# Kernel optimization log

Hardware: AMD Instinct MI355X
Metric: run time of the kernel (lower is better)

The kernel has to match this reference:

```python
import jax, jax.numpy as jnp
import numpy as np

N = 50000          # nodes
E_RAND = 800000    # random edges (avg degree 16)
D_IN = 128
H = 4              # heads (both layers)
C = 64             # per-head channels (both layers)
NEG_SLOPE = 0.2    # PyG GATConv default leaky_relu slope


def _gat_conv(x, src, dst, W, att_src, att_dst, bias, concat):
    """PyG GATConv (dropout=0, self-loops already in edge list).
    x:[N,Din] W:[Din,H*C] att_*:[H,C] bias:[H*C] or [C]."""
    n = x.shape[0]
    h = (x @ W).reshape(n, H, C)                      # [N,H,C]
    a_src = jnp.sum(h * att_src, axis=-1)             # [N,H]
    a_dst = jnp.sum(h * att_dst, axis=-1)             # [N,H]
    e = jax.nn.leaky_relu(a_src[src] + a_dst[dst], NEG_SLOPE)  # [E,H]
    # segment softmax over incoming edges of each destination node
    m = jax.ops.segment_max(e, dst, num_segments=n)    # [N,H]
    e = jnp.exp(e - m[dst])
    denom = jax.ops.segment_sum(e, dst, num_segments=n)
    alpha = e / (denom[dst] + 1e-16)                   # [E,H]
    msg = h[src] * alpha[..., None]                    # [E,H,C]
    out = jax.ops.segment_sum(msg, dst, num_segments=n)  # [N,H,C]
    if concat:
        out = out.reshape(n, H * C)
    else:
        out = out.mean(axis=1)
    return out + bias


def setup_inputs() -> dict:
    key = jax.random.key(0)
    ks = jax.random.split(key, 10)
    x = jax.random.normal(ks[0], (N, D_IN), jnp.float32)
    src = jax.random.randint(ks[1], (E_RAND,), 0, N)
    dst = jax.random.randint(ks[2], (E_RAND,), 0, N)
    loops = jnp.arange(N)  # add_self_loops=True (PyG default)
    edge_index = jnp.stack([jnp.concatenate([src, loops]),
                            jnp.concatenate([dst, loops])]).astype(jnp.int32)
    g = lambda k, shp, fan: (jax.random.normal(k, shp, jnp.float32) / np.float32(np.sqrt(fan)))
    W1 = g(ks[3], (D_IN, H * C), D_IN)
    att_src1 = g(ks[4], (H, C), C)
    att_dst1 = g(ks[5], (H, C), C)
    b1 = jnp.zeros((H * C,), jnp.float32)
    W2 = g(ks[6], (H * C, H * C), H * C)
    att_src2 = g(ks[7], (H, C), C)
    att_dst2 = g(ks[8], (H, C), C)
    b2 = jnp.zeros((C,), jnp.float32)
    return {"x": x, "edge_index": edge_index,
            "W1": W1, "att_src1": att_src1, "att_dst1": att_dst1, "b1": b1,
            "W2": W2, "att_src2": att_src2, "att_dst2": att_dst2, "b2": b2}


def reference(x, edge_index, W1, att_src1, att_dst1, b1, W2, att_src2, att_dst2, b2):
    src, dst = edge_index[0], edge_index[1]
    h = jax.nn.relu(_gat_conv(x, src, dst, W1, att_src1, att_dst1, b1, concat=True))
    h = jax.nn.relu(_gat_conv(h, src, dst, W2, att_src2, att_dst2, b2, concat=False))
    return jax.nn.softmax(h, axis=1)
```

## Files before the change

kernel.cpp:

```cpp
#include <hip/hip_runtime.h>


typedef __attribute__((ext_vector_type(8))) short short8;
typedef __attribute__((ext_vector_type(4))) float f32x4;
typedef __attribute__((ext_vector_type(2))) float f32x2;

static __device__ __forceinline__ ushort f2bf(float f) {
  uint u = __float_as_uint(f);
  return (ushort)((u + 0x7FFFu + ((u >> 16) & 1u)) >> 16);
}
static __device__ __forceinline__ float bf2f(ushort s) {
  return __uint_as_float(((uint)s) << 16);
}
static __device__ __forceinline__ unsigned char f2fp8(float f) {
  int p = __builtin_amdgcn_cvt_pk_fp8_f32(f, f, 0, false);
  return (unsigned char)(p & 0xFF);
}
static __device__ __forceinline__ uint4 cvt8bf(const float4& a, const float4& b) {
  uint4 hh;
  hh.x = (uint)f2bf(a.x) | ((uint)f2bf(a.y) << 16);
  hh.y = (uint)f2bf(a.z) | ((uint)f2bf(a.w) << 16);
  hh.z = (uint)f2bf(b.x) | ((uint)f2bf(b.y) << 16);
  hh.w = (uint)f2bf(b.z) | ((uint)f2bf(b.w) << 16);
  return hh;
}
static __device__ __forceinline__ void gl16(const ushort* g, ushort* l) {
  __builtin_amdgcn_global_load_lds(
      (const __attribute__((address_space(1))) uint*)(g),
      (__attribute__((address_space(3))) uint*)(l), 16, 0, 0);
}

__global__ __launch_bounds__(256)
void k_prep(const float* __restrict__ W1, const float* __restrict__ W2,
            ushort* __restrict__ w1t, ushort* __restrict__ w2t,
            const float* __restrict__ x, ushort* __restrict__ xb,
            int* __restrict__ cnt, int N,
            int ng , int xcb) {
  const int b = blockIdx.x;
  if (b < 128) {
    int gid = b * 256 + threadIdx.x;
    int c = gid & 255, k = gid >> 8;
    w1t[(size_t)c * 128 + k] = f2bf(W1[(size_t)k * 256 + c]);
  } else if (b < 384) {
    int gid = (b - 128) * 256 + threadIdx.x;
    int c = gid & 255, k = gid >> 8;
    w2t[(size_t)c * 256 + k] = f2bf(W2[(size_t)k * 256 + c]);
  } else if (b < 384 + xcb) {
    int i = (b - 384) * 256 + threadIdx.x;
    if (i < ng) {
      const float4* xp = (const float4*)x + (size_t)i * 2;
      float4 a = xp[0], bb = xp[1];
      ((uint4*)xb)[i] = cvt8bf(a, bb);
    }
  } else {
    int i = (b - 384 - xcb) * 1024 + threadIdx.x;
#pragma unroll
    for (int k = 0; k < 4; k++) {
      int j = i + k * 256;
      if (j < N) cnt[j] = 0;
    }
  }
}

template <int K>
static __device__ __forceinline__
void gemm_body(int bid, const ushort* __restrict__ Ah,
               const ushort* __restrict__ Bt,
               unsigned char* __restrict__ hout, int Nrows,
               const float* __restrict__ att_s, const float* __restrict__ att_d,
               float* __restrict__ a_s, float* __restrict__ a_d) {
  __shared__ ushort Asb[2][128][32];
  __shared__ ushort Bhb[2][128][32];

  const int nrb = (Nrows + 127) >> 7;
  const int rb = (bid >> 4) * 8 + (bid & 7);
  const int ch = (bid >> 3) & 1;
  if (rb >= nrb) return;
  const int row0 = rb * 128;
  const int col0 = ch * 128;

  const int t = threadIdx.x;
  const int lane = t & 63;
  const int w = t >> 6;
  const int wr = (w >> 1) * 64;
  const int wc = (w & 1) * 64;
  const int fr = lane & 15;
  const int fq = lane >> 4;

  const int srow = lane >> 2;
  const int skc = (lane & 3) * 8;
  int ar0 = row0 + w * 32 + srow;
  int ar1 = ar0 + 16;
  ar0 = ar0 < Nrows ? ar0 : Nrows - 1;
  ar1 = ar1 < Nrows ? ar1 : Nrows - 1;
  const ushort* agp0 = Ah + (size_t)ar0 * K + skc;
  const ushort* agp1 = Ah + (size_t)ar1 * K + skc;
  const ushort* bhg0 = Bt + (size_t)(col0 + w * 32 + srow) * K + skc;
  const ushort* bhg1 = bhg0 + (size_t)16 * K;

  f32x4 acc[4][4] = {};

  auto stage = [&](int buf, int k0) {
    gl16(agp0 + k0, &Asb[buf][w * 32][0]);
    gl16(agp1 + k0, &Asb[buf][w * 32 + 16][0]);
    gl16(bhg0 + k0, &Bhb[buf][w * 32][0]);
    gl16(bhg1 + k0, &Bhb[buf][w * 32 + 16][0]);
  };

  stage(0, 0);
  const int NK = K / 32;
#pragma unroll
  for (int ks = 0; ks < NK; ks++) {
    const int buf = ks & 1;
    __syncthreads();
    if (ks + 1 < NK) stage(buf ^ 1, (ks + 1) * 32);

    short8 fa[4], fbh[4];
#pragma unroll
    for (int r = 0; r < 4; r++)
      fa[r] = *(const short8*)(&Asb[buf][wr + r * 16 + fr][fq * 8]);
#pragma unroll
    for (int c = 0; c < 4; c++)
      fbh[c] = *(const short8*)(&Bhb[buf][wc + c * 16 + fr][fq * 8]);
#pragma unroll
    for (int r = 0; r < 4; r++)
#pragma unroll
      for (int c = 0; c < 4; c++)
        acc[r][c] = __builtin_amdgcn_mfma_f32_16x16x32_bf16(fa[r], fbh[c], acc[r][c], 0, 0, 0);
  }

#pragma unroll
  for (int r = 0; r < 4; r++)
#pragma unroll
    for (int c = 0; c < 4; c++) {
      int colg = col0 + wc + c * 16 + fr;
#pragma unroll
      for (int reg = 0; reg < 4; reg++) {
        int gr = row0 + wr + r * 16 + fq * 4 + reg;
        if (gr < Nrows)
          hout[(size_t)gr * 256 + colg] = f2fp8(acc[r][c][reg]);
      }
    }

  const int head = (col0 + wc) >> 6;
  float asv[4], adv[4];
#pragma unroll
  for (int c = 0; c < 4; c++) {
    asv[c] = att_s[col0 + wc + c * 16 + fr];
    adv[c] = att_d[col0 + wc + c * 16 + fr];
  }
#pragma unroll
  for (int r = 0; r < 4; r++)
#pragma unroll
    for (int reg = 0; reg < 4; reg++) {
      float ps = 0.f, pd = 0.f;
#pragma unroll
      for (int c = 0; c < 4; c++) {
        ps += acc[r][c][reg] * asv[c];
        pd += acc[r][c][reg] * adv[c];
      }
      ps += __shfl_xor(ps, 1); pd += __shfl_xor(pd, 1);
      ps += __shfl_xor(ps, 2); pd += __shfl_xor(pd, 2);
      ps += __shfl_xor(ps, 4); pd += __shfl_xor(pd, 4);
      ps += __shfl_xor(ps, 8); pd += __shfl_xor(pd, 8);
      if (fr == 0) {
        int gr = row0 + wr + r * 16 + fq * 4 + reg;
        if (gr < Nrows) {
          a_s[(size_t)gr * 4 + head] = ps;
          a_d[(size_t)gr * 4 + head] = pd;
        }
      }
    }
}

__global__ __launch_bounds__(256)
void k_gemm1_hist(const ushort* __restrict__ xb,
                  const ushort* __restrict__ Bt,
                  unsigned char* __restrict__ hout, int Nrows,
                  const float* __restrict__ att_s,
                  const float* __restrict__ att_d,
                  float* __restrict__ a_s, float* __restrict__ a_d,
                  const int* __restrict__ srcv, const int* __restrict__ dstv,
                  int* __restrict__ cnt, int* __restrict__ col2,
                  int E, int gemm_blocks) {
  if ((int)blockIdx.x < gemm_blocks) {
    gemm_body<128>(blockIdx.x, xb, Bt, hout, Nrows,
                   att_s, att_d, a_s, a_d);
  } else {
    int base = ((int)blockIdx.x - gemm_blocks) * 512 + threadIdx.x;
    int d[2], v[2], s[2];
#pragma unroll
    for (int k = 0; k < 2; k++) {
      int i = base + k * 256;
      bool ok = i < E;
      d[k] = ok ? dstv[i] : 0;
      v[k] = ok ? (srcv[i] << 8) : 0;
    }
#pragma unroll
    for (int k = 0; k < 2; k++) {
      int i = base + k * 256;
      s[k] = (i < E) ? atomicAdd(&cnt[d[k]], 1) : 64;
    }
#pragma unroll
    for (int k = 0; k < 2; k++) {
      int i = base + k * 256;
      if (i < E && s[k] < 64) col2[(d[k] << 6) + s[k]] = v[k];
    }
  }
}

__global__ __launch_bounds__(256)
void k_gemm2(const ushort* __restrict__ Ah,
             const ushort* __restrict__ Bt,
             unsigned char* __restrict__ hout, int Nrows,
             const float* __restrict__ att_s, const float* __restrict__ att_d,
             float* __restrict__ a_s, float* __restrict__ a_d) {
  gemm_body<256>(blockIdx.x, Ah, Bt, hout, Nrows,
                 att_s, att_d, a_s, a_d);
}

template <int LAYER>
__global__ __launch_bounds__(256)
void k_aggr(const unsigned char* __restrict__ hsrc,
            const int* __restrict__ cnt, const int* __restrict__ col2,
            const float* __restrict__ a_s, const float* __restrict__ a_d,
            const float* __restrict__ bias,
            ushort* __restrict__ out_h, float* __restrict__ outp, int N) {
  __shared__ int   s_sh[4][64];
  __shared__ float w_sh[4][256];
  const int wv = threadIdx.x >> 6;
  const int lane = threadIdx.x & 63;
  const int node = blockIdx.x * 4 + wv;
  if (node >= N) return;
  const int hd = lane >> 4;
  const int deg = min(cnt[node], 64);
  const int beg = node << 6;
  const float4 adst = *(const float4*)(a_d + (size_t)node * 4);

  f32x2 accA = {0.f, 0.f};
  f32x2 accB = {0.f, 0.f};
  float wsum = 0.f;
  const char* hbase = (const char*)hsrc + lane * 4;

  {
    int nc = deg;
    int off = 0;
    float4 w4 = make_float4(0.f, 0.f, 0.f, 0.f);
    if (lane < nc) {
      off = col2[beg + lane];
      const float4 a = *(const float4*)((const char*)a_s + (size_t)((uint)off >> 4));
      float e0 = a.x + adst.x; e0 = e0 > 0.f ? e0 : 0.2f * e0;
      float e1 = a.y + adst.y; e1 = e1 > 0.f ? e1 : 0.2f * e1;
      float e2 = a.z + adst.z; e2 = e2 > 0.f ? e2 : 0.2f * e2;
      float e3 = a.w + adst.w; e3 = e3 > 0.f ? e3 : 0.2f * e3;
      w4 = make_float4(__expf(e0), __expf(e1), __expf(e2), __expf(e3));
    }
    s_sh[wv][lane] = off;
    *(float4*)(&w_sh[wv][lane * 4]) = w4;
    asm volatile("s_waitcnt lgkmcnt(0)" ::: "memory");

    const float* wrow = &w_sh[wv][hd];
    const int*   srow = &s_sh[wv][0];
    int j = 0;
    for (; j + 8 <= nc; j += 8) {
      int o0 = srow[j],     o1 = srow[j + 1], o2 = srow[j + 2], o3 = srow[j + 3];
      int o4 = srow[j + 4], o5 = srow[j + 5], o6 = srow[j + 6], o7 = srow[j + 7];
      float ww0 = wrow[4 * j],      ww1 = wrow[4 * j + 4];
      float ww2 = wrow[4 * j + 8],  ww3 = wrow[4 * j + 12];
      float ww4 = wrow[4 * j + 16], ww5 = wrow[4 * j + 20];
      float ww6 = wrow[4 * j + 24], ww7 = wrow[4 * j + 28];
      uint p0 = *(const uint*)(hbase + (size_t)(uint)o0);
      uint p1 = *(const uint*)(hbase + (size_t)(uint)o1);
      uint p2 = *(const uint*)(hbase + (size_t)(uint)o2);
      uint p3 = *(const uint*)(hbase + (size_t)(uint)o3);
      uint p4 = *(const uint*)(hbase + (size_t)(uint)o4);
      uint p5 = *(const uint*)(hbase + (size_t)(uint)o5);
      uint p6 = *(const uint*)(hbase + (size_t)(uint)o6);
      uint p7 = *(const uint*)(hbase + (size_t)(uint)o7);
      wsum += ww0 + ww1 + ww2 + ww3;
      wsum += ww4 + ww5 + ww6 + ww7;
      f32x2 W;
#define EDGE_FMA(ww, p)                                                     \
      {                                                                     \
        f32x2 lo = __builtin_amdgcn_cvt_pk_f32_fp8((p), false);             \
        f32x2 hi = __builtin_amdgcn_cvt_pk_f32_fp8((p), true);              \
        W.x = (ww); W.y = (ww);                                             \
        accA = __builtin_elementwise_fma(W, lo, accA);                      \
        accB = __builtin_elementwise_fma(W, hi, accB);                      \
      }
      EDGE_FMA(ww0, p0) EDGE_FMA(ww1, p1) EDGE_FMA(ww2, p2) EDGE_FMA(ww3, p3)
      EDGE_FMA(ww4, p4) EDGE_FMA(ww5, p5) EDGE_FMA(ww6, p6) EDGE_FMA(ww7, p7)
    }
    for (; j + 4 <= nc; j += 4) {
      int o0 = srow[j], o1 = srow[j + 1], o2 = srow[j + 2], o3 = srow[j + 3];
      float ww0 = wrow[4 * j],     ww1 = wrow[4 * j + 4];
      float ww2 = wrow[4 * j + 8], ww3 = wrow[4 * j + 12];
      uint p0 = *(const uint*)(hbase + (size_t)(uint)o0);
      uint p1 = *(const uint*)(hbase + (size_t)(uint)o1);
      uint p2 = *(const uint*)(hbase + (size_t)(uint)o2);
      uint p3 = *(const uint*)(hbase + (size_t)(uint)o3);
      wsum += ww0 + ww1 + ww2 + ww3;
      f32x2 W;
      EDGE_FMA(ww0, p0) EDGE_FMA(ww1, p1) EDGE_FMA(ww2, p2) EDGE_FMA(ww3, p3)
    }
    for (; j < nc; j++) {
      int o = srow[j];
      float ww = wrow[4 * j];
      uint p = *(const uint*)(hbase + (size_t)(uint)o);
      wsum += ww;
      f32x2 W;
      EDGE_FMA(ww, p)
    }
#undef EDGE_FMA
  }

  float inv = 1.0f / wsum;
  float4 v = make_float4(accA.x * inv, accA.y * inv, accB.x * inv, accB.y * inv);

  if (LAYER == 1) {
    const float4 bv = *(const float4*)(bias + lane * 4);
    v.x = fmaxf(v.x + bv.x, 0.f);
    v.y = fmaxf(v.y + bv.y, 0.f);
    v.z = fmaxf(v.z + bv.z, 0.f);
    v.w = fmaxf(v.w + bv.w, 0.f);
    ushort4 h;
    h.x = f2bf(v.x); h.y = f2bf(v.y); h.z = f2bf(v.z); h.w = f2bf(v.w);
    *(ushort4*)(out_h + (size_t)node * 256 + lane * 4) = h;
  } else {
    v.x += __shfl_xor(v.x, 16); v.y += __shfl_xor(v.y, 16);
    v.z += __shfl_xor(v.z, 16); v.w += __shfl_xor(v.w, 16);
    v.x += __shfl_xor(v.x, 32); v.y += __shfl_xor(v.y, 32);
    v.z += __shfl_xor(v.z, 32); v.w += __shfl_xor(v.w, 32);
    const int c4 = (lane & 15) * 4;
    const float4 bv = *(const float4*)(bias + c4);
    v.x = fmaxf(v.x * 0.25f + bv.x, 0.f);
    v.y = fmaxf(v.y * 0.25f + bv.y, 0.f);
    v.z = fmaxf(v.z * 0.25f + bv.z, 0.f);
    v.w = fmaxf(v.w * 0.25f + bv.w, 0.f);
    float mx = fmaxf(fmaxf(v.x, v.y), fmaxf(v.z, v.w));
    for (int off = 8; off >= 1; off >>= 1) mx = fmaxf(mx, __shfl_xor(mx, off));
    v.x = __expf(v.x - mx); v.y = __expf(v.y - mx);
    v.z = __expf(v.z - mx); v.w = __expf(v.w - mx);
    float sum = v.x + v.y + v.z + v.w;
    for (int off = 8; off >= 1; off >>= 1) sum += __shfl_xor(sum, off);
    float is = 1.0f / sum;
    v.x *= is; v.y *= is; v.z *= is; v.w *= is;
    if (lane < 16) *(float4*)(outp + (size_t)node * 64 + c4) = v;
  }
}


extern "C" void kernel_launch(void* const* d_in, const int* in_sizes, int n_in,
                              void* d_out, int out_size, void* d_ws, size_t ws_size,
                              hipStream_t stream) {
  const float* x   = (const float*)d_in[0];
  const int*   ei  = (const int*)d_in[1];
  const float* W1  = (const float*)d_in[2];
  const float* as1 = (const float*)d_in[3];
  const float* ad1 = (const float*)d_in[4];
  const float* b1  = (const float*)d_in[5];
  const float* W2  = (const float*)d_in[6];
  const float* as2 = (const float*)d_in[7];
  const float* ad2 = (const float*)d_in[8];
  const float* b2  = (const float*)d_in[9];
  float* out = (float*)d_out;

  const int N = in_sizes[0] / 128;
  const int E = in_sizes[1] / 2;
  const int* srcv = ei;
  const int* dstv = ei + E;

  unsigned char* h8 = (unsigned char*)d_ws;
  ushort* hb   = (ushort*)(h8 + (size_t)N * 256);
  ushort* w1t  = hb + (size_t)N * 256;
  ushort* w2t  = w1t + 256 * 128;
  float*  zbuf = (float*)(w2t + 256 * 256);
  float* a_s1 = zbuf;
  float* a_d1 = a_s1 + (size_t)N * 4;
  float* a_s2 = a_d1 + (size_t)N * 4;
  float* a_d2 = a_s2 + (size_t)N * 4;
  int* cnt    = (int*)(zbuf + (size_t)N * 16);
  int* col2   = cnt + N;
  ushort* xb  = (ushort*)(col2 + (size_t)N * 64);

  const int eb2 = (E + 511) / 512;
  const int ng = N * 16;
  const int xcb = (ng + 255) / 256;
  const int zb  = (N + 1023) / 1024;

  const int nrb = (N + 127) / 128;
  const int gemm_blocks = ((nrb + 7) / 8) * 16;
  const int wb = (N + 3) / 4;

  k_prep<<<384 + xcb + zb, 256, 0, stream>>>(W1, W2, w1t, w2t,
                                             x, xb, cnt, N, ng, xcb);
  k_gemm1_hist<<<gemm_blocks + eb2, 256, 0, stream>>>(
      xb, w1t, h8, N, as1, ad1, a_s1, a_d1,
      srcv, dstv, cnt, col2, E, gemm_blocks);
  k_aggr<1><<<wb, 256, 0, stream>>>(h8, cnt, col2, a_s1, a_d1, b1,
                                    hb, nullptr, N);
  k_gemm2<<<gemm_blocks, 256, 0, stream>>>(hb, w2t, h8, N,
                                           as2, ad2, a_s2, a_d2);
  k_aggr<2><<<wb, 256, 0, stream>>>(h8, cnt, col2, a_s2, a_d2, b2,
                                    nullptr, out, N);
}
```

Before: 253.1 us.

## Split edge histogram into atomic slot pass in prep and scatter pass in gemm1

New measurement: 252.5 us. About the same (-0.2%).

```diff
diff --git a/kernel.cpp b/kernel.cpp
--- a/kernel.cpp
+++ b/kernel.cpp
@@ -31,12 +31,14 @@
 }
 
 __global__ __launch_bounds__(256)
-void k_prep(const float* __restrict__ W1, const float* __restrict__ W2,
-            ushort* __restrict__ w1t, ushort* __restrict__ w2t,
-            const float* __restrict__ x, ushort* __restrict__ xb,
-            int* __restrict__ cnt, int N,
-            int ng , int xcb) {
+void k_prep_hist(const float* __restrict__ W1, const float* __restrict__ W2,
+                 ushort* __restrict__ w1t, ushort* __restrict__ w2t,
+                 const int* __restrict__ dstv, int* __restrict__ cnt,
+                 int* __restrict__ pe, int E,
+                 const float* __restrict__ x, ushort* __restrict__ xb,
+                 int ng) {
   const int b = blockIdx.x;
+  const int eb = (E + 255) >> 8;
   if (b < 128) {
     int gid = b * 256 + threadIdx.x;
     int c = gid & 255, k = gid >> 8;
@@ -45,19 +47,15 @@
     int gid = (b - 128) * 256 + threadIdx.x;
     int c = gid & 255, k = gid >> 8;
     w2t[(size_t)c * 256 + k] = f2bf(W2[(size_t)k * 256 + c]);
-  } else if (b < 384 + xcb) {
+  } else if (b < 384 + eb) {
     int i = (b - 384) * 256 + threadIdx.x;
+    if (i < E) pe[i] = atomicAdd(&cnt[dstv[i]], 1);
+  } else {
+    int i = (b - 384 - eb) * 256 + threadIdx.x;
     if (i < ng) {
       const float4* xp = (const float4*)x + (size_t)i * 2;
       float4 a = xp[0], bb = xp[1];
       ((uint4*)xb)[i] = cvt8bf(a, bb);
-    }
-  } else {
-    int i = (b - 384 - xcb) * 1024 + threadIdx.x;
-#pragma unroll
-    for (int k = 0; k < 4; k++) {
-      int j = i + k * 256;
-      if (j < N) cnt[j] = 0;
     }
   }
 }
@@ -174,37 +172,27 @@
 }
 
 __global__ __launch_bounds__(256)
-void k_gemm1_hist(const ushort* __restrict__ xb,
-                  const ushort* __restrict__ Bt,
-                  unsigned char* __restrict__ hout, int Nrows,
-                  const float* __restrict__ att_s,
-                  const float* __restrict__ att_d,
-                  float* __restrict__ a_s, float* __restrict__ a_d,
-                  const int* __restrict__ srcv, const int* __restrict__ dstv,
-                  int* __restrict__ cnt, int* __restrict__ col2,
-                  int E, int gemm_blocks) {
+void k_gemm1_scatter(const ushort* __restrict__ xb,
+                     const ushort* __restrict__ Bt,
+                     unsigned char* __restrict__ hout, int Nrows,
+                     const float* __restrict__ att_s,
+                     const float* __restrict__ att_d,
+                     float* __restrict__ a_s, float* __restrict__ a_d,
+                     const int* __restrict__ srcv, const int* __restrict__ dstv,
+                     const int* __restrict__ pe, int* __restrict__ col2,
+                     int E, int gemm_blocks) {
   if ((int)blockIdx.x < gemm_blocks) {
     gemm_body<128>(blockIdx.x, xb, Bt, hout, Nrows,
                    att_s, att_d, a_s, a_d);
   } else {
-    int base = ((int)blockIdx.x - gemm_blocks) * 512 + threadIdx.x;
-    int d[2], v[2], s[2];
-#pragma unroll
-    for (int k = 0; k < 2; k++) {
+    int base = ((int)blockIdx.x - gemm_blocks) * 1024 + threadIdx.x;
+#pragma unroll
+    for (int k = 0; k < 4; k++) {
       int i = base + k * 256;
-      bool ok = i < E;
-      d[k] = ok ? dstv[i] : 0;
-      v[k] = ok ? (srcv[i] << 8) : 0;
-    }
-#pragma unroll
-    for (int k = 0; k < 2; k++) {
-      int i = base + k * 256;
-      s[k] = (i < E) ? atomicAdd(&cnt[d[k]], 1) : 64;
-    }
-#pragma unroll
-    for (int k = 0; k < 2; k++) {
-      int i = base + k * 256;
-      if (i < E && s[k] < 64) col2[(d[k] << 6) + s[k]] = v[k];
+      if (i < E) {
+        int s = pe[i];
+        if (s < 64) col2[(dstv[i] << 6) + s] = srcv[i] << 8;
+      }
     }
   }
 }
@@ -381,22 +369,24 @@
   float* a_d2 = a_s2 + (size_t)N * 4;
   int* cnt    = (int*)(zbuf + (size_t)N * 16);
   int* col2   = cnt + N;
-  ushort* xb  = (ushort*)(col2 + (size_t)N * 64);
-
-  const int eb2 = (E + 511) / 512;
+  int* pe     = col2 + (size_t)N * 64;
+  ushort* xb  = (ushort*)(pe + E);
+
+  const int eb  = (E + 255) / 256;
+  const int eb4 = (E + 1023) / 1024;
   const int ng = N * 16;
   const int xcb = (ng + 255) / 256;
-  const int zb  = (N + 1023) / 1024;
 
   const int nrb = (N + 127) / 128;
   const int gemm_blocks = ((nrb + 7) / 8) * 16;
   const int wb = (N + 3) / 4;
 
-  k_prep<<<384 + xcb + zb, 256, 0, stream>>>(W1, W2, w1t, w2t,
-                                             x, xb, cnt, N, ng, xcb);
-  k_gemm1_hist<<<gemm_blocks + eb2, 256, 0, stream>>>(
+  hipMemsetAsync(cnt, 0, (size_t)N * 4, stream);
+  k_prep_hist<<<384 + eb + xcb, 256, 0, stream>>>(
+      W1, W2, w1t, w2t, dstv, cnt, pe, E, x, xb, ng);
+  k_gemm1_scatter<<<gemm_blocks + eb4, 256, 0, stream>>>(
       xb, w1t, h8, N, as1, ad1, a_s1, a_d1,
-      srcv, dstv, cnt, col2, E, gemm_blocks);
+      srcv, dstv, pe, col2, E, gemm_blocks);
   k_aggr<1><<<wb, 256, 0, stream>>>(h8, cnt, col2, a_s1, a_d1, b1,
                                     hb, nullptr, N);
   k_gemm2<<<gemm_blocks, 256, 0, stream>>>(hb, w2t, h8, N,
```
